# Performance work log

Hardware: AMD Instinct MI355X
Metric: run time of the kernel (lower is better)

The kernel has to match this reference:

```python
import jax, jax.numpy as jnp
import numpy as np

N_NODES = 100000
N_EDGES = 1600000
EPS = 1e-5


def _xavier(key, shape):
    fan_out, fan_in = shape
    lim = float(np.sqrt(6.0 / (fan_in + fan_out)))
    return jax.random.uniform(key, shape, jnp.float32, -lim, lim)


def setup_inputs() -> dict:
    key = jax.random.key(0)
    ks = jax.random.split(key, 16)
    d_in, d1, d2, d3 = 32, 64, 128, 64
    inp = {
        "x": jax.random.normal(ks[0], (N_NODES, d_in), jnp.float32),
        "edge_index": jax.random.randint(ks[1], (2, N_EDGES), 0, N_NODES, jnp.int64),
        "edge_weight": jax.random.uniform(ks[2], (N_EDGES,), jnp.float32),
        # GraphConv params: lin_rel (with bias) applied to aggregated msgs, lin_root (no bias)
        "W1_rel": _xavier(ks[3], (d1, d_in)), "b1": jnp.zeros((d1,), jnp.float32), "W1_root": _xavier(ks[4], (d1, d_in)),
        "W2_rel": _xavier(ks[5], (d2, d1)), "b2": jnp.zeros((d2,), jnp.float32), "W2_root": _xavier(ks[6], (d2, d1)),
        "W3_rel": _xavier(ks[7], (d3, d2)), "b3": jnp.zeros((d3,), jnp.float32), "W3_root": _xavier(ks[8], (d3, d2)),
        # BatchNorm affine params
        "g1": jnp.ones((d1,), jnp.float32), "be1": jnp.zeros((d1,), jnp.float32),
        "g2": jnp.ones((d2,), jnp.float32), "be2": jnp.zeros((d2,), jnp.float32),
        "g3": jnp.ones((d3,), jnp.float32), "be3": jnp.zeros((d3,), jnp.float32),
        # node-level classifier: Linear(64,32) -> ReLU -> Linear(32,2)
        "Wc1": _xavier(ks[9], (32, d3)), "bc1": jnp.zeros((32,), jnp.float32),
        "Wc2": _xavier(ks[10], (2, 32)), "bc2": jnp.zeros((2,), jnp.float32),
    }
    return inp


def _graph_conv(x, src, dst, W_rel, b, W_root, ew=None):
    msg = x[src]                      # [E, d] gather
    if ew is not None:
        msg = msg * ew[:, None]
    agg = jax.ops.segment_sum(msg, dst, num_segments=N_NODES)  # [N, d] scatter-add
    return agg @ W_rel.T + b + x @ W_root.T


def _bn(h, g, beta):
    mu = jnp.mean(h, axis=0)
    var = jnp.var(h, axis=0)
    return (h - mu) * jax.lax.rsqrt(var + EPS) * g + beta


def reference(x, edge_index, edge_weight,
              W1_rel, b1, W1_root, W2_rel, b2, W2_root, W3_rel, b3, W3_root,
              g1, be1, g2, be2, g3, be3, Wc1, bc1, Wc2, bc2):
    src, dst = edge_index[0], edge_index[1]
    h1 = jax.nn.relu(_bn(_graph_conv(x, src, dst, W1_rel, b1, W1_root), g1, be1))
    h2 = jax.nn.relu(_bn(_graph_conv(h1, src, dst, W2_rel, b2, W2_root), g2, be2))
    h3 = _bn(_graph_conv(h2, src, dst, W3_rel, b3, W3_root, edge_weight), g3, be3)
    h3 = jax.nn.relu(h3 + h1)  # residual (dims match, no projection)
    logits = jax.nn.relu(h3 @ Wc1.T + bc1) @ Wc2.T + bc2  # [N, 2]
    return logits
```

## Files before the change

### kernel.cpp

```cpp
#include <hip/hip_runtime.h>

#define N_NODES 100000
#define N_EDGES 1600000
#define EPSV 1e-5f

__device__ __forceinline__ ushort f2bf(float f) {
  unsigned u = __float_as_uint(f);
  unsigned r = (u + 0x7FFFu + ((u >> 16) & 1u)) >> 16;
  return (ushort)r;
}


#define FILL_SUB 256
#define GRP_W 12500

__global__ void hist_kernel(const int* __restrict__ ei, int* __restrict__ cnt) {
  const int g = blockIdx.x & 7;
  const int sub = blockIdx.x >> 3;
  const int lo = g * GRP_W, hi = lo + GRP_W;
  const int EPB = (N_EDGES + FILL_SUB - 1) / FILL_SUB;
  const int beg = sub * EPB;
  const int end = min(beg + EPB, N_EDGES);
  for (int e = beg + (int)threadIdx.x; e < end; e += (int)blockDim.x) {
    int d = __builtin_nontemporal_load(ei + N_EDGES + e);
    if (d >= lo && d < hi) atomicAdd(&cnt[d], 1);
  }
}

#define SCAN_BLK 1024
#define SCAN_NB ((N_NODES + SCAN_BLK - 1) / SCAN_BLK)

__global__ void scan_phase1(const int* __restrict__ cnt, int* __restrict__ blocksum) {
  __shared__ int part[256];
  int base = blockIdx.x * SCAN_BLK + threadIdx.x * 4;
  int s = 0;
#pragma unroll
  for (int i = 0; i < 4; ++i) {
    int idx = base + i;
    if (idx < N_NODES) s += cnt[idx];
  }
  part[threadIdx.x] = s;
  __syncthreads();
  for (int d = 128; d > 0; d >>= 1) {
    if (threadIdx.x < d) part[threadIdx.x] += part[threadIdx.x + d];
    __syncthreads();
  }
  if (threadIdx.x == 0) blocksum[blockIdx.x] = part[0];
}

__global__ void scan_phase2(int* __restrict__ blocksum, int* __restrict__ rowptr) {
  __shared__ int part[128];
  int tid = threadIdx.x;
  int v = (tid < SCAN_NB) ? blocksum[tid] : 0;
  part[tid] = v;
  __syncthreads();
  for (int d = 1; d < 128; d <<= 1) {
    int t = (tid >= d) ? part[tid - d] : 0;
    __syncthreads();
    part[tid] += t;
    __syncthreads();
  }
  if (tid < SCAN_NB) blocksum[tid] = part[tid] - v;
  if (tid == 127) rowptr[N_NODES] = part[127];
}

__global__ void scan_phase3(const int* __restrict__ cnt, const int* __restrict__ blocksum,
                            int* __restrict__ rowptr, int* __restrict__ cursor) {
  __shared__ int part[256];
  int base = blockIdx.x * SCAN_BLK + threadIdx.x * 4;
  int c[4];
  int s = 0;
#pragma unroll
  for (int i = 0; i < 4; ++i) {
    int idx = base + i;
    c[i] = (idx < N_NODES) ? cnt[idx] : 0;
    s += c[i];
  }
  part[threadIdx.x] = s;
  __syncthreads();
  int me = s;
  for (int d = 1; d < 256; d <<= 1) {
    int t = (threadIdx.x >= d) ? part[threadIdx.x - d] : 0;
    __syncthreads();
    part[threadIdx.x] += t;
    __syncthreads();
  }
  int off = blocksum[blockIdx.x] + part[threadIdx.x] - me;
#pragma unroll
  for (int i = 0; i < 4; ++i) {
    int idx = base + i;
    if (idx < N_NODES) {
      rowptr[idx] = off;
      cursor[idx] = off;
      off += c[i];
    }
  }
}

__global__ void fill_kernel(const int* __restrict__ ei, const float* __restrict__ ew,
                            int* __restrict__ cursor, unsigned* __restrict__ col) {
  const int g = blockIdx.x & 7;
  const int sub = blockIdx.x >> 3;
  const int lo = g * GRP_W, hi = lo + GRP_W;
  const int EPB = (N_EDGES + FILL_SUB - 1) / FILL_SUB;
  const int beg = sub * EPB;
  const int end = min(beg + EPB, N_EDGES);
  for (int e = beg + (int)threadIdx.x; e < end; e += (int)blockDim.x) {
    int d = __builtin_nontemporal_load(ei + N_EDGES + e);
    if (d < lo || d >= hi) continue;
    int p = atomicAdd(&cursor[d], 1);
    int src = __builtin_nontemporal_load(ei + e);
    float w = __builtin_nontemporal_load(ew + e);
    col[p] = ((unsigned)f2bf(w) << 17) | (unsigned)src;
  }
}


__global__ void cast_bf16(const float* __restrict__ in, ushort* __restrict__ out, int n4) {
  int i = blockIdx.x * blockDim.x + threadIdx.x;
  if (i >= n4) return;
  float4 v = reinterpret_cast<const float4*>(in)[i];
  ushort4 o = make_ushort4(f2bf(v.x), f2bf(v.y), f2bf(v.z), f2bf(v.w));
  reinterpret_cast<ushort4*>(out)[i] = o;
}


__global__ void wtrans_kernel(const float* __restrict__ W1rel, const float* __restrict__ W1root,
                              const float* __restrict__ W2rel, const float* __restrict__ W2root,
                              const float* __restrict__ W3rel, const float* __restrict__ W3root,
                              float* __restrict__ Wt) {
  int i = blockIdx.x * blockDim.x + threadIdx.x;
  if (i >= 36864) return;
  float v;
  if (i < 4096) {
    int k = i >> 6, j = i & 63;
    v = (k < 32) ? W1rel[j * 32 + k] : W1root[j * 32 + (k - 32)];
  } else if (i < 20480) {
    int r = i - 4096;
    int k = r >> 7, j = r & 127;
    v = (k < 64) ? W2rel[j * 64 + k] : W2root[j * 64 + (k - 64)];
  } else if (i < 28672) {
    int r = i - 20480;
    int k = r >> 6, j = r & 63;
    v = W3rel[j * 128 + k];
  } else {
    int r = i - 28672;
    int k = r >> 6, j = r & 63;
    v = W3root[j * 128 + k];
  }
  Wt[i] = v;
}


#define SRC_OF(v) ((v) & 0x1FFFFu)
#define W_OF(v) __uint_as_float(((v) >> 17) << 16)

__device__ __forceinline__ unsigned pack2bf(float a, float b) {
  return (unsigned)f2bf(a) | ((unsigned)f2bf(b) << 16);
}

__global__ void gather_d32_bf(const ushort* __restrict__ xb, const int* __restrict__ rowptr,
                              const unsigned* __restrict__ col, ushort* __restrict__ agg) {
  int gid = blockIdx.x * blockDim.x + threadIdx.x;
  int n = gid >> 2;
  if (n >= N_NODES) return;
  int c = gid & 3;
  int beg = rowptr[n], end = rowptr[n + 1];
  float acc[8];
#pragma unroll
  for (int i = 0; i < 8; ++i) acc[i] = 0.f;
  int p = beg;
  for (; p + 1 < end; p += 2) {
    unsigned e0 = col[p], e1 = col[p + 1];
    uint4 u0 = *reinterpret_cast<const uint4*>(xb + (size_t)SRC_OF(e0) * 32 + c * 8);
    uint4 u1 = *reinterpret_cast<const uint4*>(xb + (size_t)SRC_OF(e1) * 32 + c * 8);
    unsigned a0[4] = {u0.x, u0.y, u0.z, u0.w};
    unsigned a1[4] = {u1.x, u1.y, u1.z, u1.w};
#pragma unroll
    for (int i = 0; i < 4; ++i) {
      acc[2 * i]     += __uint_as_float(a0[i] << 16) + __uint_as_float(a1[i] << 16);
      acc[2 * i + 1] += __uint_as_float(a0[i] & 0xFFFF0000u) +
                        __uint_as_float(a1[i] & 0xFFFF0000u);
    }
  }
  if (p < end) {
    unsigned e0 = col[p];
    uint4 u0 = *reinterpret_cast<const uint4*>(xb + (size_t)SRC_OF(e0) * 32 + c * 8);
    unsigned a0[4] = {u0.x, u0.y, u0.z, u0.w};
#pragma unroll
    for (int i = 0; i < 4; ++i) {
      acc[2 * i]     += __uint_as_float(a0[i] << 16);
      acc[2 * i + 1] += __uint_as_float(a0[i] & 0xFFFF0000u);
    }
  }
  uint4 o = make_uint4(pack2bf(acc[0], acc[1]), pack2bf(acc[2], acc[3]),
                       pack2bf(acc[4], acc[5]), pack2bf(acc[6], acc[7]));
  *reinterpret_cast<uint4*>(agg + (size_t)n * 32 + c * 8) = o;
}

template <bool WEIGHTED, bool TRANS, bool OUTB16>
__global__ void gather_d64_bf(const ushort* __restrict__ hb, const int* __restrict__ rowptr,
                              const unsigned* __restrict__ col,
                              const float* __restrict__ sc, const float* __restrict__ sh,
                              void* __restrict__ aggv) {
  int gid = blockIdx.x * blockDim.x + threadIdx.x;
  int n = gid >> 3;
  if (n >= N_NODES) return;
  int c = gid & 7;
  int beg = rowptr[n], end = rowptr[n + 1];
  float sc8[8], sh8[8];
  if (TRANS) {
#pragma unroll
    for (int i = 0; i < 8; ++i) {
      sc8[i] = sc[c * 8 + i];
      sh8[i] = sh[c * 8 + i];
    }
  }
  float acc[8];
#pragma unroll
  for (int i = 0; i < 8; ++i) acc[i] = 0.f;

  auto body = [&](unsigned ev, const uint4& u) {
    float w = WEIGHTED ? W_OF(ev) : 1.f;
    unsigned uu[4] = {u.x, u.y, u.z, u.w};
#pragma unroll
    for (int i = 0; i < 4; ++i) {
      float lo = __uint_as_float(uu[i] << 16);
      float hi = __uint_as_float(uu[i] & 0xFFFF0000u);
      if (TRANS) {
        lo = fmaxf(fmaf(lo, sc8[2 * i], sh8[2 * i]), 0.f);
        hi = fmaxf(fmaf(hi, sc8[2 * i + 1], sh8[2 * i + 1]), 0.f);
      }
      if (WEIGHTED) {
        acc[2 * i]     = fmaf(lo, w, acc[2 * i]);
        acc[2 * i + 1] = fmaf(hi, w, acc[2 * i + 1]);
      } else {
        acc[2 * i]     += lo;
        acc[2 * i + 1] += hi;
      }
    }
  };

  int p = beg;
  for (; p + 1 < end; p += 2) {
    unsigned e0 = col[p], e1 = col[p + 1];
    uint4 u0 = *reinterpret_cast<const uint4*>(hb + (size_t)SRC_OF(e0) * 64 + c * 8);
    uint4 u1 = *reinterpret_cast<const uint4*>(hb + (size_t)SRC_OF(e1) * 64 + c * 8);
    body(e0, u0);
    body(e1, u1);
  }
  if (p < end) {
    unsigned e0 = col[p];
    uint4 u0 = *reinterpret_cast<const uint4*>(hb + (size_t)SRC_OF(e0) * 64 + c * 8);
    body(e0, u0);
  }
  if constexpr (OUTB16) {
    uint4 o = make_uint4(pack2bf(acc[0], acc[1]), pack2bf(acc[2], acc[3]),
                         pack2bf(acc[4], acc[5]), pack2bf(acc[6], acc[7]));
    *reinterpret_cast<uint4*>((ushort*)aggv + (size_t)n * 64 + c * 8) = o;
  } else {
    float* op = (float*)aggv + (size_t)n * 64 + c * 8;
    *reinterpret_cast<float4*>(op)     = make_float4(acc[0], acc[1], acc[2], acc[3]);
    *reinterpret_cast<float4*>(op + 4) = make_float4(acc[4], acc[5], acc[6], acc[7]);
  }
}


template <int K1, int K2, int DO, int A1B16, int A2B16, int TA1, int TA2, int RADD,
          int STATS, int OUTM>
__global__ __launch_bounds__(256, 4) void gemm_node(
    const void* __restrict__ A1v, const void* __restrict__ A2v,
    const float* __restrict__ Wt,
    const float* __restrict__ sc, const float* __restrict__ sh,
    const float* __restrict__ R, float* __restrict__ out, ushort* __restrict__ outb,
    float* __restrict__ sums) {
  constexpr int K = K1 + K2;
  constexpr int NC = K / 32;
  constexpr int NJB = DO / 64;
  __shared__ __align__(16) float A_lds[64][36];
  __shared__ __align__(16) float W_lds[32][DO];

  const int tid = threadIdx.x;
  const int tx = tid & 15, ty = tid >> 4;
  const int nbase = blockIdx.x * 64;

  float4 acc[4][NJB];
#pragma unroll
  for (int i = 0; i < 4; ++i)
#pragma unroll
    for (int jb = 0; jb < NJB; ++jb) acc[i][jb] = make_float4(0.f, 0.f, 0.f, 0.f);

#pragma unroll 1
  for (int c = 0; c < NC; ++c) {
    const int kb = c * 32;
    if (c) __syncthreads();
#pragma unroll
    for (int it = 0; it < 2; ++it) {
      int idx = it * 256 + tid;
      int nl = idx >> 3;
      int kq = (idx & 7) * 4;
      int k = kb + kq;
      int ng = nbase + nl;
      float4 v = make_float4(0.f, 0.f, 0.f, 0.f);
      bool isA1 = (K2 == 0) || (k < K1);
      if (ng < N_NODES) {
        if (isA1) {
          if constexpr (A1B16) {
            uint2 u = *reinterpret_cast<const uint2*>(
                (const ushort*)A1v + (size_t)ng * K1 + k);
            v.x = __uint_as_float(u.x << 16);
            v.y = __uint_as_float(u.x & 0xFFFF0000u);
            v.z = __uint_as_float(u.y << 16);
            v.w = __uint_as_float(u.y & 0xFFFF0000u);
          } else {
            v = *reinterpret_cast<const float4*>((const float*)A1v + (size_t)ng * K1 + k);
          }
        } else {
          if constexpr (A2B16) {
            uint2 u = *reinterpret_cast<const uint2*>(
                (const ushort*)A2v + (size_t)ng * K2 + (k - K1));
            v.x = __uint_as_float(u.x << 16);
            v.y = __uint_as_float(u.x & 0xFFFF0000u);
            v.z = __uint_as_float(u.y << 16);
            v.w = __uint_as_float(u.y & 0xFFFF0000u);
          } else {
            v = *reinterpret_cast<const float4*>(
                (const float*)A2v + (size_t)ng * K2 + (k - K1));
          }
        }
      }
      if constexpr (TA1) {
        if (isA1) {
          float4 s4 = *reinterpret_cast<const float4*>(sc + k);
          float4 h4 = *reinterpret_cast<const float4*>(sh + k);
          v.x = fmaxf(fmaf(v.x, s4.x, h4.x), 0.f);
          v.y = fmaxf(fmaf(v.y, s4.y, h4.y), 0.f);
          v.z = fmaxf(fmaf(v.z, s4.z, h4.z), 0.f);
          v.w = fmaxf(fmaf(v.w, s4.w, h4.w), 0.f);
        }
      }
      if constexpr (TA2 && K2 > 0) {
        if (!isA1) {
          float4 s4 = *reinterpret_cast<const float4*>(sc + (k - K1));
          float4 h4 = *reinterpret_cast<const float4*>(sh + (k - K1));
          v.x = fmaxf(fmaf(v.x, s4.x, h4.x), 0.f);
          v.y = fmaxf(fmaf(v.y, s4.y, h4.y), 0.f);
          v.z = fmaxf(fmaf(v.z, s4.z, h4.z), 0.f);
          v.w = fmaxf(fmaf(v.w, s4.w, h4.w), 0.f);
        }
      }
      *reinterpret_cast<float4*>(&A_lds[nl][kq]) = v;
    }
    {
      const float4* wsrc = reinterpret_cast<const float4*>(Wt + (size_t)kb * DO);
      float4* wdst = reinterpret_cast<float4*>(&W_lds[0][0]);
#pragma unroll
      for (int it = 0; it < DO / 32; ++it)
        wdst[it * 256 + tid] = wsrc[it * 256 + tid];
    }
    __syncthreads();
#pragma unroll 2
    for (int k4 = 0; k4 < 8; ++k4) {
      float4 a[4];
#pragma unroll
      for (int i = 0; i < 4; ++i)
        a[i] = *reinterpret_cast<const float4*>(&A_lds[ty * 4 + i][k4 * 4]);
#pragma unroll
      for (int q = 0; q < 4; ++q) {
#pragma unroll
        for (int jb = 0; jb < NJB; ++jb) {
          float4 w = *reinterpret_cast<const float4*>(&W_lds[k4 * 4 + q][jb * 64 + tx * 4]);
#pragma unroll
          for (int i = 0; i < 4; ++i) {
            float av = reinterpret_cast<const float*>(&a[i])[q];
            acc[i][jb].x = fmaf(av, w.x, acc[i][jb].x);
            acc[i][jb].y = fmaf(av, w.y, acc[i][jb].y);
            acc[i][jb].z = fmaf(av, w.z, acc[i][jb].z);
            acc[i][jb].w = fmaf(av, w.w, acc[i][jb].w);
          }
        }
      }
    }
  }
#pragma unroll
  for (int i = 0; i < 4; ++i) {
    int ng = nbase + ty * 4 + i;
    if (ng >= N_NODES) continue;
#pragma unroll
    for (int jb = 0; jb < NJB; ++jb) {
      if constexpr (RADD) {
        float4 rr = *reinterpret_cast<const float4*>(R + (size_t)ng * DO + jb * 64 + tx * 4);
        acc[i][jb].x += rr.x; acc[i][jb].y += rr.y;
        acc[i][jb].z += rr.z; acc[i][jb].w += rr.w;
      }
      size_t off = (size_t)ng * DO + jb * 64 + tx * 4;
      if constexpr (OUTM == 1) {
        ushort4 o = make_ushort4(f2bf(acc[i][jb].x), f2bf(acc[i][jb].y),
                                 f2bf(acc[i][jb].z), f2bf(acc[i][jb].w));
        *reinterpret_cast<ushort4*>((ushort*)out + off) = o;
      } else {
        *reinterpret_cast<float4*>(out + off) = acc[i][jb];
        if constexpr (OUTM == 2) {
          ushort4 o = make_ushort4(f2bf(acc[i][jb].x), f2bf(acc[i][jb].y),
                                   f2bf(acc[i][jb].z), f2bf(acc[i][jb].w));
          *reinterpret_cast<ushort4*>(outb + off) = o;
        }
      }
    }
  }
  if constexpr (STATS) {
    __syncthreads();
    float* sums_l = &A_lds[0][0];
    float* sq_l = &W_lds[0][0];
#pragma unroll
    for (int jb = 0; jb < NJB; ++jb) {
      float4 s = make_float4(0.f, 0.f, 0.f, 0.f);
      float4 q = make_float4(0.f, 0.f, 0.f, 0.f);
#pragma unroll
      for (int i = 0; i < 4; ++i) {
        if (nbase + ty * 4 + i < N_NODES) {
          float4 v = acc[i][jb];
          s.x += v.x; s.y += v.y; s.z += v.z; s.w += v.w;
          q.x = fmaf(v.x, v.x, q.x); q.y = fmaf(v.y, v.y, q.y);
          q.z = fmaf(v.z, v.z, q.z); q.w = fmaf(v.w, v.w, q.w);
        }
      }
      *reinterpret_cast<float4*>(&sums_l[ty * DO + jb * 64 + tx * 4]) = s;
      *reinterpret_cast<float4*>(&sq_l[ty * DO + jb * 64 + tx * 4]) = q;
    }
    __syncthreads();
    if (tid < DO) {
      float s = 0.f, q = 0.f;
#pragma unroll
      for (int t = 0; t < 16; ++t) {
        s += sums_l[t * DO + tid];
        q += sq_l[t * DO + tid];
      }
      unsafeAtomicAdd(&sums[tid], s);
      unsafeAtomicAdd(&sums[DO + tid], q);
    }
  }
}


__global__ void bn_finalize(const float* __restrict__ sums, const float* __restrict__ g,
                            const float* __restrict__ be, float* __restrict__ sc,
                            float* __restrict__ sh, int D) {
  int j = threadIdx.x;
  if (j >= D) return;
  const float invN = 1.f / (float)N_NODES;
  float mean = sums[j] * invN;
  float var = sums[D + j] * invN - mean * mean;
  float r = rsqrtf(var + EPSV);
  float scale = g[j] * r;
  sc[j] = scale;
  sh[j] = be[j] - mean * scale;
}


__global__ __launch_bounds__(256) void final_fused(
    const float* __restrict__ h3p, const float* __restrict__ h1p,
    const float* __restrict__ sc1, const float* __restrict__ sh1,
    const float* __restrict__ sc3, const float* __restrict__ sh3,
    const float* __restrict__ Wc1, const float* __restrict__ bc1,
    const float* __restrict__ Wc2, const float* __restrict__ bc2,
    float* __restrict__ out) {
  __shared__ __align__(16) float t_lds[64][68];
  __shared__ __align__(16) float w1_lds[64][36];
  __shared__ __align__(16) float c_lds[64][36];
  __shared__ __align__(16) float w2_lds[64];
  __shared__ __align__(16) float b1_lds[32];
  __shared__ float b2_lds[2];
  const int tid = threadIdx.x;
  const int nbase = blockIdx.x * 64;

#pragma unroll
  for (int it = 0; it < 4; ++it) {
    int idx = it * 256 + tid;
    int nl = idx >> 4;
    int k = (idx & 15) * 4;
    int ng = nbase + nl;
    float4 v = make_float4(0.f, 0.f, 0.f, 0.f);
    if (ng < N_NODES) {
      float4 p = *reinterpret_cast<const float4*>(h3p + (size_t)ng * 64 + k);
      float4 u = *reinterpret_cast<const float4*>(h1p + (size_t)ng * 64 + k);
      float4 sa = *reinterpret_cast<const float4*>(sc1 + k);
      float4 ha = *reinterpret_cast<const float4*>(sh1 + k);
      float4 sb = *reinterpret_cast<const float4*>(sc3 + k);
      float4 hb = *reinterpret_cast<const float4*>(sh3 + k);
      float h1x = fmaxf(fmaf(u.x, sa.x, ha.x), 0.f);
      float h1y = fmaxf(fmaf(u.y, sa.y, ha.y), 0.f);
      float h1z = fmaxf(fmaf(u.z, sa.z, ha.z), 0.f);
      float h1w = fmaxf(fmaf(u.w, sa.w, ha.w), 0.f);
      v.x = fmaxf(fmaf(p.x, sb.x, hb.x) + h1x, 0.f);
      v.y = fmaxf(fmaf(p.y, sb.y, hb.y) + h1y, 0.f);
      v.z = fmaxf(fmaf(p.z, sb.z, hb.z) + h1z, 0.f);
      v.w = fmaxf(fmaf(p.w, sb.w, hb.w) + h1w, 0.f);
    }
    *reinterpret_cast<float4*>(&t_lds[nl][k]) = v;
  }
#pragma unroll
  for (int it = 0; it < 8; ++it) {
    int idx = it * 256 + tid;
    int j = idx >> 6;
    int k = idx & 63;
    w1_lds[k][j] = Wc1[(size_t)j * 64 + k];
  }
  if (tid < 64) w2_lds[tid] = Wc2[tid];
  else if (tid < 96) b1_lds[tid - 64] = bc1[tid - 64];
  else if (tid < 98) b2_lds[tid - 96] = bc2[tid - 96];
  __syncthreads();

  {
    const int tx = tid & 7, ty = tid >> 3;
    float4 a0c = make_float4(0.f, 0.f, 0.f, 0.f);
    float4 a1c = make_float4(0.f, 0.f, 0.f, 0.f);
#pragma unroll 4
    for (int k4 = 0; k4 < 16; ++k4) {
      float4 a0 = *reinterpret_cast<const float4*>(&t_lds[ty * 2 + 0][k4 * 4]);
      float4 a1 = *reinterpret_cast<const float4*>(&t_lds[ty * 2 + 1][k4 * 4]);
#pragma unroll
      for (int q = 0; q < 4; ++q) {
        float4 w = *reinterpret_cast<const float4*>(&w1_lds[k4 * 4 + q][tx * 4]);
        float a0q = reinterpret_cast<const float*>(&a0)[q];
        float a1q = reinterpret_cast<const float*>(&a1)[q];
        a0c.x = fmaf(a0q, w.x, a0c.x); a0c.y = fmaf(a0q, w.y, a0c.y);
        a0c.z = fmaf(a0q, w.z, a0c.z); a0c.w = fmaf(a0q, w.w, a0c.w);
        a1c.x = fmaf(a1q, w.x, a1c.x); a1c.y = fmaf(a1q, w.y, a1c.y);
        a1c.z = fmaf(a1q, w.z, a1c.z); a1c.w = fmaf(a1q, w.w, a1c.w);
      }
    }
    float4 b = *reinterpret_cast<const float4*>(&b1_lds[tx * 4]);
    a0c.x = fmaxf(a0c.x + b.x, 0.f); a0c.y = fmaxf(a0c.y + b.y, 0.f);
    a0c.z = fmaxf(a0c.z + b.z, 0.f); a0c.w = fmaxf(a0c.w + b.w, 0.f);
    a1c.x = fmaxf(a1c.x + b.x, 0.f); a1c.y = fmaxf(a1c.y + b.y, 0.f);
    a1c.z = fmaxf(a1c.z + b.z, 0.f); a1c.w = fmaxf(a1c.w + b.w, 0.f);
    *reinterpret_cast<float4*>(&c_lds[ty * 2 + 0][tx * 4]) = a0c;
    *reinterpret_cast<float4*>(&c_lds[ty * 2 + 1][tx * 4]) = a1c;
  }
  __syncthreads();

  if (tid < 128) {
    int nl = tid >> 1, o = tid & 1;
    int ng = nbase + nl;
    if (ng < N_NODES) {
      float s = b2_lds[o];
#pragma unroll
      for (int k = 0; k < 32; ++k) s = fmaf(c_lds[nl][k], w2_lds[o * 32 + k], s);
      out[(size_t)ng * 2 + o] = s;
    }
  }
}


extern "C" void kernel_launch(void* const* d_in, const int* in_sizes, int n_in,
                              void* d_out, int out_size, void* d_ws, size_t ws_size,
                              hipStream_t stream) {
  const float* x      = (const float*)d_in[0];
  const int*   ei     = (const int*)d_in[1];
  const float* ew     = (const float*)d_in[2];
  const float* W1rel  = (const float*)d_in[3];
  const float* W1root = (const float*)d_in[5];
  const float* W2rel  = (const float*)d_in[6];
  const float* W2root = (const float*)d_in[8];
  const float* W3rel  = (const float*)d_in[9];
  const float* W3root = (const float*)d_in[11];
  const float* g1  = (const float*)d_in[12];
  const float* be1 = (const float*)d_in[13];
  const float* g2  = (const float*)d_in[14];
  const float* be2 = (const float*)d_in[15];
  const float* g3  = (const float*)d_in[16];
  const float* be3 = (const float*)d_in[17];
  const float* Wc1 = (const float*)d_in[18];
  const float* bc1 = (const float*)d_in[19];
  const float* Wc2 = (const float*)d_in[20];
  const float* bc2 = (const float*)d_in[21];

  float* ws = (float*)d_ws;
  const size_t NF = (size_t)N_NODES * 64;
  float* A = ws;
  float* B = ws + NF;
  float* C = ws + 2 * NF;
  float* E = ws + 3 * NF;
  float* X = ws + 5 * NF;
  float* S = X;
  int* rowptr   = (int*)(X + 1024);
  int* cnt      = rowptr + (N_NODES + 2);
  int* cursor   = cnt + N_NODES;
  int* blocksum = cursor + N_NODES;
  unsigned* col = (unsigned*)(blocksum + 128);
  float* Wt     = (float*)(col + N_EDGES);
  float* Wt1  = Wt;
  float* Wt2  = Wt + 4096;
  float* Wt3r = Wt + 20480;
  float* Wt3o = Wt + 28672;

  ushort* agg1b  = (ushort*)A;
  ushort* agg2b  = (ushort*)A;
  ushort* xb     = (ushort*)B;
  ushort* y2b    = (ushort*)B;
  ushort* h1preb = (ushort*)E;
  ushort* h2preb = (ushort*)E;

  hipMemsetAsync(S, 0, 1024 * sizeof(float), stream);
  hipMemsetAsync(cnt, 0, N_NODES * sizeof(int), stream);

  const int tileBlocks = (N_NODES + 63) / 64;

  cast_bf16<<<(N_NODES * 32 / 4 + 255) / 256, 256, 0, stream>>>(x, xb, N_NODES * 32 / 4);
  wtrans_kernel<<<144, 256, 0, stream>>>(W1rel, W1root, W2rel, W2root, W3rel, W3root, Wt);

  hist_kernel<<<8 * FILL_SUB, 256, 0, stream>>>(ei, cnt);
  scan_phase1<<<SCAN_NB, 256, 0, stream>>>(cnt, blocksum);
  scan_phase2<<<1, 128, 0, stream>>>(blocksum, rowptr);
  scan_phase3<<<SCAN_NB, 256, 0, stream>>>(cnt, blocksum, rowptr, cursor);
  fill_kernel<<<8 * FILL_SUB, 256, 0, stream>>>(ei, ew, cursor, col);

  gather_d32_bf<<<(N_NODES * 4 + 255) / 256, 256, 0, stream>>>(xb, rowptr, col, agg1b);
  gemm_node<32, 32, 64, 1, 1, 0, 0, 0, 1, 2><<<tileBlocks, 256, 0, stream>>>(
      agg1b, xb, Wt1, nullptr, nullptr, nullptr, C, h1preb, S);
  bn_finalize<<<1, 128, 0, stream>>>(S, g1, be1, S + 128, S + 192, 64);

  gather_d64_bf<false, true, true><<<(N_NODES * 8 + 255) / 256, 256, 0, stream>>>(
      h1preb, rowptr, col, S + 128, S + 192, agg2b);
  gemm_node<64, 64, 128, 1, 0, 0, 1, 0, 1, 1><<<tileBlocks, 256, 0, stream>>>(
      agg2b, C, Wt2, S + 128, S + 192, nullptr, (float*)h2preb, nullptr, S + 256);
  bn_finalize<<<1, 128, 0, stream>>>(S + 256, g2, be2, S + 512, S + 640, 128);

  gemm_node<128, 0, 64, 1, 0, 1, 0, 0, 0, 1><<<tileBlocks, 256, 0, stream>>>(
      h2preb, nullptr, Wt3r, S + 512, S + 640, nullptr, (float*)y2b, nullptr, nullptr);

  gather_d64_bf<true, false, false><<<(N_NODES * 8 + 255) / 256, 256, 0, stream>>>(
      y2b, rowptr, col, nullptr, nullptr, A);
  gemm_node<128, 0, 64, 1, 0, 1, 0, 1, 1, 0><<<tileBlocks, 256, 0, stream>>>(
      h2preb, nullptr, Wt3o, S + 512, S + 640, A, B, nullptr, S + 768);
  bn_finalize<<<1, 128, 0, stream>>>(S + 768, g3, be3, S + 896, S + 960, 64);

  final_fused<<<tileBlocks, 256, 0, stream>>>(B, C, S + 128, S + 192, S + 896, S + 960,
                                              Wc1, bc1, Wc2, bc2, (float*)d_out);
}
```

Before: 475.2 us.

## Pre-bucket edges by destination group to avoid repeated full edge scans

Adds a bucket kernel that reads each edge once, packs the destination with its bf16 weight and source, and appends it to one of eight per-group buckets using block-local counting. The histogram and CSR fill kernels then read only their own bucket instead of scanning the whole edge list eight times and discarding out-of-range entries. This trades redundant edge reads for one extra write and read of 8-byte bucket entries. It relies on a fixed bucket capacity that holds for roughly uniform destinations and on extra workspace after the weight area.

After: 499.4 us. +5.1%, slower.

```diff
diff --git a/kernel.cpp b/kernel.cpp
--- a/kernel.cpp
+++ b/kernel.cpp
@@ -13,17 +13,60 @@
 
 #define FILL_SUB 256
 #define GRP_W 12500
-
-__global__ void hist_kernel(const int* __restrict__ ei, int* __restrict__ cnt) {
+#define BUCKET_CAP 210000
+
+__global__ __launch_bounds__(256) void bucket_kernel(const int* __restrict__ ei,
+                                                     const float* __restrict__ ew,
+                                                     int* __restrict__ bcur,
+                                                     unsigned long long* __restrict__ bkt) {
+  __shared__ int lcnt[8];
+  __shared__ int lbase[8];
+  const int tid = threadIdx.x;
+  if (tid < 8) lcnt[tid] = 0;
+  __syncthreads();
+  int d[7];
+  unsigned pay[7];
+  int g[7];
+  const int base_t = blockIdx.x * 256 + tid;
+  const int STRIDE = 1024 * 256;
+#pragma unroll
+  for (int it = 0; it < 7; ++it) {
+    int e = base_t + it * STRIDE;
+    if (e < N_EDGES) {
+      d[it] = __builtin_nontemporal_load(ei + N_EDGES + e);
+      int src = __builtin_nontemporal_load(ei + e);
+      float w = __builtin_nontemporal_load(ew + e);
+      pay[it] = ((unsigned)f2bf(w) << 17) | (unsigned)src;
+      g[it] = d[it] / GRP_W;
+      atomicAdd(&lcnt[g[it]], 1);
+    } else {
+      g[it] = -1;
+    }
+  }
+  __syncthreads();
+  if (tid < 8) lbase[tid] = atomicAdd(&bcur[tid * 16], lcnt[tid]);
+  __syncthreads();
+  if (tid < 8) lcnt[tid] = 0;
+  __syncthreads();
+#pragma unroll
+  for (int it = 0; it < 7; ++it) {
+    if (g[it] >= 0) {
+      int off = atomicAdd(&lcnt[g[it]], 1);
+      bkt[(size_t)g[it] * BUCKET_CAP + lbase[g[it]] + off] =
+          ((unsigned long long)pay[it] << 32) | (unsigned)(unsigned)d[it];
+    }
+  }
+}
+
+__global__ void hist_kernel(const unsigned long long* __restrict__ bkt,
+                            const int* __restrict__ bcur, int* __restrict__ cnt) {
   const int g = blockIdx.x & 7;
   const int sub = blockIdx.x >> 3;
-  const int lo = g * GRP_W, hi = lo + GRP_W;
-  const int EPB = (N_EDGES + FILL_SUB - 1) / FILL_SUB;
-  const int beg = sub * EPB;
-  const int end = min(beg + EPB, N_EDGES);
-  for (int e = beg + (int)threadIdx.x; e < end; e += (int)blockDim.x) {
-    int d = __builtin_nontemporal_load(ei + N_EDGES + e);
-    if (d >= lo && d < hi) atomicAdd(&cnt[d], 1);
+  const int total = bcur[g * 16];
+  const unsigned long long* b = bkt + (size_t)g * BUCKET_CAP;
+  for (int i = sub * 256 + (int)threadIdx.x; i < total; i += FILL_SUB * 256) {
+    unsigned long long ev = __builtin_nontemporal_load(b + i);
+    atomicAdd(&cnt[(unsigned)ev], 1);
   }
 }
 
@@ -97,21 +140,19 @@
   }
 }
 
-__global__ void fill_kernel(const int* __restrict__ ei, const float* __restrict__ ew,
-                            int* __restrict__ cursor, unsigned* __restrict__ col) {
+__global__ void fill_kernel(const unsigned long long* __restrict__ bkt,
+                            const int* __restrict__ bcur, int* __restrict__ cursor,
+                            unsigned* __restrict__ col) {
   const int g = blockIdx.x & 7;
   const int sub = blockIdx.x >> 3;
-  const int lo = g * GRP_W, hi = lo + GRP_W;
-  const int EPB = (N_EDGES + FILL_SUB - 1) / FILL_SUB;
-  const int beg = sub * EPB;
-  const int end = min(beg + EPB, N_EDGES);
-  for (int e = beg + (int)threadIdx.x; e < end; e += (int)blockDim.x) {
-    int d = __builtin_nontemporal_load(ei + N_EDGES + e);
-    if (d < lo || d >= hi) continue;
+  const int total = bcur[g * 16];
+  const unsigned long long* b = bkt + (size_t)g * BUCKET_CAP;
+  for (int i = sub * 256 + (int)threadIdx.x; i < total; i += FILL_SUB * 256) {
+    unsigned long long ev = __builtin_nontemporal_load(b + i);
+    unsigned d = (unsigned)ev;
+    unsigned payload = (unsigned)(ev >> 32);
     int p = atomicAdd(&cursor[d], 1);
-    int src = __builtin_nontemporal_load(ei + e);
-    float w = __builtin_nontemporal_load(ew + e);
-    col[p] = ((unsigned)f2bf(w) << 17) | (unsigned)src;
+    col[p] = payload;
   }
 }
 
@@ -588,8 +629,10 @@
   int* cnt      = rowptr + (N_NODES + 2);
   int* cursor   = cnt + N_NODES;
   int* blocksum = cursor + N_NODES;
-  unsigned* col = (unsigned*)(blocksum + 128);
+  int* bcur     = blocksum + 128;
+  unsigned* col = (unsigned*)(bcur + 130);
   float* Wt     = (float*)(col + N_EDGES);
+  unsigned long long* bkt = (unsigned long long*)(Wt + 36864);
   float* Wt1  = Wt;
   float* Wt2  = Wt + 4096;
   float* Wt3r = Wt + 20480;
@@ -604,17 +647,19 @@
 
   hipMemsetAsync(S, 0, 1024 * sizeof(float), stream);
   hipMemsetAsync(cnt, 0, N_NODES * sizeof(int), stream);
+  hipMemsetAsync(bcur, 0, 128 * sizeof(int), stream);
 
   const int tileBlocks = (N_NODES + 63) / 64;
 
   cast_bf16<<<(N_NODES * 32 / 4 + 255) / 256, 256, 0, stream>>>(x, xb, N_NODES * 32 / 4);
   wtrans_kernel<<<144, 256, 0, stream>>>(W1rel, W1root, W2rel, W2root, W3rel, W3root, Wt);
 
-  hist_kernel<<<8 * FILL_SUB, 256, 0, stream>>>(ei, cnt);
+  bucket_kernel<<<1024, 256, 0, stream>>>(ei, ew, bcur, bkt);
+  hist_kernel<<<8 * FILL_SUB, 256, 0, stream>>>(bkt, bcur, cnt);
   scan_phase1<<<SCAN_NB, 256, 0, stream>>>(cnt, blocksum);
   scan_phase2<<<1, 128, 0, stream>>>(blocksum, rowptr);
   scan_phase3<<<SCAN_NB, 256, 0, stream>>>(cnt, blocksum, rowptr, cursor);
-  fill_kernel<<<8 * FILL_SUB, 256, 0, stream>>>(ei, ew, cursor, col);
+  fill_kernel<<<8 * FILL_SUB, 256, 0, stream>>>(bkt, bcur, cursor, col);
 
   gather_d32_bf<<<(N_NODES * 4 + 255) / 256, 256, 0, stream>>>(xb, rowptr, col, agg1b);
   gemm_node<32, 32, 64, 1, 1, 0, 0, 0, 1, 2><<<tileBlocks, 256, 0, stream>>>(
```

## Unroll gather loops by four and keep h1 pre-activation only in bf16

Applied to the files above, without the earlier changes.

The gather kernels now issue four independent row loads per iteration instead of two, to raise memory-level parallelism on the random neighbour reads. The layer-1 GEMM no longer writes both an fp32 and a bf16 copy of h1. It writes only the bf16 copy, and layer 2's root GEMM input and the final residual read that bf16 buffer. This cuts write and read traffic, but the residual path now uses bf16-rounded h1 where it used fp32, which slightly changes accuracy.

Result: no change. 471.6 us (-0.7%).

```diff
diff --git a/kernel.cpp b/kernel.cpp
--- a/kernel.cpp
+++ b/kernel.cpp
@@ -169,29 +169,29 @@
   float acc[8];
 #pragma unroll
   for (int i = 0; i < 8; ++i) acc[i] = 0.f;
+
+  auto body = [&](const uint4& u) {
+    unsigned uu[4] = {u.x, u.y, u.z, u.w};
+#pragma unroll
+    for (int i = 0; i < 4; ++i) {
+      acc[2 * i]     += __uint_as_float(uu[i] << 16);
+      acc[2 * i + 1] += __uint_as_float(uu[i] & 0xFFFF0000u);
+    }
+  };
+
   int p = beg;
-  for (; p + 1 < end; p += 2) {
-    unsigned e0 = col[p], e1 = col[p + 1];
+  for (; p + 3 < end; p += 4) {
+    unsigned e0 = col[p], e1 = col[p + 1], e2 = col[p + 2], e3 = col[p + 3];
     uint4 u0 = *reinterpret_cast<const uint4*>(xb + (size_t)SRC_OF(e0) * 32 + c * 8);
     uint4 u1 = *reinterpret_cast<const uint4*>(xb + (size_t)SRC_OF(e1) * 32 + c * 8);
-    unsigned a0[4] = {u0.x, u0.y, u0.z, u0.w};
-    unsigned a1[4] = {u1.x, u1.y, u1.z, u1.w};
-#pragma unroll
-    for (int i = 0; i < 4; ++i) {
-      acc[2 * i]     += __uint_as_float(a0[i] << 16) + __uint_as_float(a1[i] << 16);
-      acc[2 * i + 1] += __uint_as_float(a0[i] & 0xFFFF0000u) +
-                        __uint_as_float(a1[i] & 0xFFFF0000u);
-    }
-  }
-  if (p < end) {
+    uint4 u2 = *reinterpret_cast<const uint4*>(xb + (size_t)SRC_OF(e2) * 32 + c * 8);
+    uint4 u3 = *reinterpret_cast<const uint4*>(xb + (size_t)SRC_OF(e3) * 32 + c * 8);
+    body(u0); body(u1); body(u2); body(u3);
+  }
+  for (; p < end; ++p) {
     unsigned e0 = col[p];
     uint4 u0 = *reinterpret_cast<const uint4*>(xb + (size_t)SRC_OF(e0) * 32 + c * 8);
-    unsigned a0[4] = {u0.x, u0.y, u0.z, u0.w};
-#pragma unroll
-    for (int i = 0; i < 4; ++i) {
-      acc[2 * i]     += __uint_as_float(a0[i] << 16);
-      acc[2 * i + 1] += __uint_as_float(a0[i] & 0xFFFF0000u);
-    }
+    body(u0);
   }
   uint4 o = make_uint4(pack2bf(acc[0], acc[1]), pack2bf(acc[2], acc[3]),
                        pack2bf(acc[4], acc[5]), pack2bf(acc[6], acc[7]));
@@ -242,14 +242,15 @@
   };
 
   int p = beg;
-  for (; p + 1 < end; p += 2) {
-    unsigned e0 = col[p], e1 = col[p + 1];
+  for (; p + 3 < end; p += 4) {
+    unsigned e0 = col[p], e1 = col[p + 1], e2 = col[p + 2], e3 = col[p + 3];
     uint4 u0 = *reinterpret_cast<const uint4*>(hb + (size_t)SRC_OF(e0) * 64 + c * 8);
     uint4 u1 = *reinterpret_cast<const uint4*>(hb + (size_t)SRC_OF(e1) * 64 + c * 8);
-    body(e0, u0);
-    body(e1, u1);
-  }
-  if (p < end) {
+    uint4 u2 = *reinterpret_cast<const uint4*>(hb + (size_t)SRC_OF(e2) * 64 + c * 8);
+    uint4 u3 = *reinterpret_cast<const uint4*>(hb + (size_t)SRC_OF(e3) * 64 + c * 8);
+    body(e0, u0); body(e1, u1); body(e2, u2); body(e3, u3);
+  }
+  for (; p < end; ++p) {
     unsigned e0 = col[p];
     uint4 u0 = *reinterpret_cast<const uint4*>(hb + (size_t)SRC_OF(e0) * 64 + c * 8);
     body(e0, u0);
@@ -459,7 +460,7 @@
 
 
 __global__ __launch_bounds__(256) void final_fused(
-    const float* __restrict__ h3p, const float* __restrict__ h1p,
+    const float* __restrict__ h3p, const ushort* __restrict__ h1p,
     const float* __restrict__ sc1, const float* __restrict__ sh1,
     const float* __restrict__ sc3, const float* __restrict__ sh3,
     const float* __restrict__ Wc1, const float* __restrict__ bc1,
@@ -483,15 +484,19 @@
     float4 v = make_float4(0.f, 0.f, 0.f, 0.f);
     if (ng < N_NODES) {
       float4 p = *reinterpret_cast<const float4*>(h3p + (size_t)ng * 64 + k);
-      float4 u = *reinterpret_cast<const float4*>(h1p + (size_t)ng * 64 + k);
+      uint2 uu = *reinterpret_cast<const uint2*>(h1p + (size_t)ng * 64 + k);
+      float ux = __uint_as_float(uu.x << 16);
+      float uy = __uint_as_float(uu.x & 0xFFFF0000u);
+      float uz = __uint_as_float(uu.y << 16);
+      float uw = __uint_as_float(uu.y & 0xFFFF0000u);
       float4 sa = *reinterpret_cast<const float4*>(sc1 + k);
       float4 ha = *reinterpret_cast<const float4*>(sh1 + k);
       float4 sb = *reinterpret_cast<const float4*>(sc3 + k);
       float4 hb = *reinterpret_cast<const float4*>(sh3 + k);
-      float h1x = fmaxf(fmaf(u.x, sa.x, ha.x), 0.f);
-      float h1y = fmaxf(fmaf(u.y, sa.y, ha.y), 0.f);
-      float h1z = fmaxf(fmaf(u.z, sa.z, ha.z), 0.f);
-      float h1w = fmaxf(fmaf(u.w, sa.w, ha.w), 0.f);
+      float h1x = fmaxf(fmaf(ux, sa.x, ha.x), 0.f);
+      float h1y = fmaxf(fmaf(uy, sa.y, ha.y), 0.f);
+      float h1z = fmaxf(fmaf(uz, sa.z, ha.z), 0.f);
+      float h1w = fmaxf(fmaf(uw, sa.w, ha.w), 0.f);
       v.x = fmaxf(fmaf(p.x, sb.x, hb.x) + h1x, 0.f);
       v.y = fmaxf(fmaf(p.y, sb.y, hb.y) + h1y, 0.f);
       v.z = fmaxf(fmaf(p.z, sb.z, hb.z) + h1z, 0.f);
@@ -599,7 +604,7 @@
   ushort* agg2b  = (ushort*)A;
   ushort* xb     = (ushort*)B;
   ushort* y2b    = (ushort*)B;
-  ushort* h1preb = (ushort*)E;
+  ushort* h1preb = (ushort*)C;
   ushort* h2preb = (ushort*)E;
 
   hipMemsetAsync(S, 0, 1024 * sizeof(float), stream);
@@ -617,14 +622,14 @@
   fill_kernel<<<8 * FILL_SUB, 256, 0, stream>>>(ei, ew, cursor, col);
 
   gather_d32_bf<<<(N_NODES * 4 + 255) / 256, 256, 0, stream>>>(xb, rowptr, col, agg1b);
-  gemm_node<32, 32, 64, 1, 1, 0, 0, 0, 1, 2><<<tileBlocks, 256, 0, stream>>>(
-      agg1b, xb, Wt1, nullptr, nullptr, nullptr, C, h1preb, S);
+  gemm_node<32, 32, 64, 1, 1, 0, 0, 0, 1, 1><<<tileBlocks, 256, 0, stream>>>(
+      agg1b, xb, Wt1, nullptr, nullptr, nullptr, (float*)h1preb, nullptr, S);
   bn_finalize<<<1, 128, 0, stream>>>(S, g1, be1, S + 128, S + 192, 64);
 
   gather_d64_bf<false, true, true><<<(N_NODES * 8 + 255) / 256, 256, 0, stream>>>(
       h1preb, rowptr, col, S + 128, S + 192, agg2b);
-  gemm_node<64, 64, 128, 1, 0, 0, 1, 0, 1, 1><<<tileBlocks, 256, 0, stream>>>(
-      agg2b, C, Wt2, S + 128, S + 192, nullptr, (float*)h2preb, nullptr, S + 256);
+  gemm_node<64, 64, 128, 1, 1, 0, 1, 0, 1, 1><<<tileBlocks, 256, 0, stream>>>(
+      agg2b, h1preb, Wt2, S + 128, S + 192, nullptr, (float*)h2preb, nullptr, S + 256);
   bn_finalize<<<1, 128, 0, stream>>>(S + 256, g2, be2, S + 512, S + 640, 128);
 
   gemm_node<128, 0, 64, 1, 0, 1, 0, 0, 0, 1><<<tileBlocks, 256, 0, stream>>>(
@@ -636,6 +641,6 @@
       h2preb, nullptr, Wt3o, S + 512, S + 640, A, B, nullptr, S + 768);
   bn_finalize<<<1, 128, 0, stream>>>(S + 768, g3, be3, S + 896, S + 960, 64);
 
-  final_fused<<<tileBlocks, 256, 0, stream>>>(B, C, S + 128, S + 192, S + 896, S + 960,
+  final_fused<<<tileBlocks, 256, 0, stream>>>(B, h1preb, S + 128, S + 192, S + 896, S + 960,
                                               Wc1, bc1, Wc2, bc2, (float*)d_out);
 }
```
